# Optimization experiments

Hardware: AMD Instinct MI355X
Metric: run time of the kernel (lower is better)

Reference implementation:

```python
import jax, jax.numpy as jnp
import numpy as np

N_NODES = 50000
N_EDGES = 800000
IN_FEATS, H_FEATS, N_CLASSES = 64, 64, 16


def setup_inputs() -> dict:
    key = jax.random.key(0)
    ks = jax.random.split(key, 8)
    x = jax.random.normal(ks[0], (N_NODES, IN_FEATS), dtype=jnp.float32)
    src = jax.random.randint(ks[1], (N_EDGES,), 0, N_NODES, dtype=jnp.int64)
    dst = jax.random.randint(ks[2], (N_EDGES,), 0, N_NODES, dtype=jnp.int64)
    W_self1 = jax.random.normal(ks[3], (IN_FEATS, H_FEATS), dtype=jnp.float32) / np.sqrt(IN_FEATS)
    W_neigh1 = jax.random.normal(ks[4], (IN_FEATS, H_FEATS), dtype=jnp.float32) / np.sqrt(IN_FEATS)
    b1 = jnp.zeros((H_FEATS,), dtype=jnp.float32)
    W_self2 = jax.random.normal(ks[5], (H_FEATS, N_CLASSES), dtype=jnp.float32) / np.sqrt(H_FEATS)
    W_neigh2 = jax.random.normal(ks[6], (H_FEATS, N_CLASSES), dtype=jnp.float32) / np.sqrt(H_FEATS)
    b2 = jnp.zeros((N_CLASSES,), dtype=jnp.float32)
    return {"x": x, "src": src, "dst": dst,
            "W_self1": W_self1, "W_neigh1": W_neigh1, "b1": b1,
            "W_self2": W_self2, "W_neigh2": W_neigh2, "b2": b2}


def _mean_agg(h, src, dst, n_nodes):
    # gather source-node features along edges, sum into destinations, divide by in-degree
    summed = jax.ops.segment_sum(h[src], dst, num_segments=n_nodes)  # [N, d]
    deg = jax.ops.segment_sum(jnp.ones_like(src, dtype=h.dtype), dst, num_segments=n_nodes)
    return summed / jnp.maximum(deg, 1.0)[:, None]  # zero in-degree -> zeros (DGL semantics)


def _sage_layer(h, src, dst, W_self, W_neigh, b):
    h_neigh = _mean_agg(h, src, dst, h.shape[0])
    return h @ W_self + h_neigh @ W_neigh + b


def reference(x, src, dst, W_self1, W_neigh1, b1, W_self2, W_neigh2, b2):
    h = _sage_layer(x, src, dst, W_self1, W_neigh1, b1)
    h = jax.nn.relu(h)
    out = _sage_layer(h, src, dst, W_self2, W_neigh2, b2)
    return out
```

## Files before the change

kernel.cpp:

```cpp
#include <hip/hip_runtime.h>
#include <hip/hip_bf16.h>
#include <cstring>


#define FEATS 64
#define CLS   16
#define EPT   16
#define CAP   5120
#define CAPN  64

typedef unsigned short bf16_t;
typedef float floatx2 __attribute__((ext_vector_type(2)));

__device__ __forceinline__ float bfbits2f(unsigned lo16) {
    unsigned v = lo16 << 16;
    float f;
    __builtin_memcpy(&f, &v, 4);
    return f;
}
__device__ __forceinline__ bf16_t f2bf(float f) {
    unsigned u;
    __builtin_memcpy(&u, &f, 4);
    u = (u + 0x7FFFu + ((u >> 16) & 1u)) >> 16;
    return (bf16_t)u;
}
__device__ __forceinline__ unsigned pack2(float a, float b) {
    return (unsigned)f2bf(a) | ((unsigned)f2bf(b) << 16);
}
__device__ __forceinline__ unsigned pack4_fp8(float a, float b, float c, float d) {
    int q = __builtin_amdgcn_cvt_pk_fp8_f32(a, b, 0, false);
    q = __builtin_amdgcn_cvt_pk_fp8_f32(c, d, q, true);
    return (unsigned)q;
}

__global__ __launch_bounds__(256) void fused_pg_kernel(
    const int* __restrict__ src, const int* __restrict__ dst,
    int* __restrict__ bucket_cnt, int* __restrict__ epart, int E,
    const float* __restrict__ x, const float* __restrict__ Ws,
    const float* __restrict__ Wn, bf16_t* __restrict__ selfo,
    unsigned char* __restrict__ t1, int N, int nbp)
{
    __shared__ float smem[16512];
    int t = threadIdx.x;

    if ((int)blockIdx.x < nbp) {
        int* hist = (int*)smem;
        int* base = hist + 256;
        int e0 = blockIdx.x * (256 * EPT);
        hist[t] = 0;
        __syncthreads();
        int pk[EPT];
        int bk[EPT];
#pragma unroll
        for (int j = 0; j < EPT; ++j) {
            int e = e0 + j * 256 + t;
            if (e < E) {
                int d = dst[e];
                pk[j] = (src[e] << 8) | (d & 255);
                bk[j] = d >> 8;
                atomicAdd(&hist[bk[j]], 1);
            } else bk[j] = -1;
        }
        __syncthreads();
        int c = hist[t];
        if (c) base[t] = atomicAdd(&bucket_cnt[t], c);
        hist[t] = 0;
        __syncthreads();
#pragma unroll
        for (int j = 0; j < EPT; ++j) {
            if (bk[j] >= 0) {
                int r = atomicAdd(&hist[bk[j]], 1);
                epart[bk[j] * CAP + base[bk[j]] + r] = pk[j];
            }
        }
        return;
    }

    float* Wc = smem;
    float* xs = smem + 8192;
    int node0 = ((int)blockIdx.x - nbp) * 128;

    for (int idx = t; idx < 64 * 128; idx += 256) {
        int k = idx >> 7, c = idx & 127;
        Wc[idx] = (c < 64) ? Ws[k * 64 + c] : Wn[k * 64 + (c - 64)];
    }
    for (int idx = t; idx < 128 * 16; idx += 256) {
        int row = idx >> 4, c4 = idx & 15;
        int node = node0 + row;
        float4 v = (node < N) ? ((const float4*)(x + (size_t)node * 64))[c4]
                              : make_float4(0.f, 0.f, 0.f, 0.f);
        float* p = &xs[row * 65 + c4 * 4];
        p[0] = v.x; p[1] = v.y; p[2] = v.z; p[3] = v.w;
    }
    __syncthreads();

    int m = t & 31;
    int g = t >> 5;
    float acc[4][16];
#pragma unroll
    for (int j = 0; j < 4; ++j)
#pragma unroll
        for (int c = 0; c < 16; ++c) acc[j][c] = 0.f;

    for (int k = 0; k < 64; ++k) {
        float w[16];
        const float* wp = &Wc[k * 128 + g * 16];
#pragma unroll
        for (int c = 0; c < 16; ++c) w[c] = wp[c];
        float a0 = xs[m * 65 + k];
        float a1 = xs[(m + 32) * 65 + k];
        float a2 = xs[(m + 64) * 65 + k];
        float a3 = xs[(m + 96) * 65 + k];
#pragma unroll
        for (int c = 0; c < 16; ++c) {
            acc[0][c] += a0 * w[c];
            acc[1][c] += a1 * w[c];
            acc[2][c] += a2 * w[c];
            acc[3][c] += a3 * w[c];
        }
    }
#pragma unroll
    for (int j = 0; j < 4; ++j) {
        int node = node0 + m + 32 * j;
        if (node < N) {
            if (g < 4) {
                bf16_t* dstp = selfo + (size_t)node * 64 + g * 16;
                uint4 p0, p1;
                p0.x = pack2(acc[j][0],  acc[j][1]);  p0.y = pack2(acc[j][2],  acc[j][3]);
                p0.z = pack2(acc[j][4],  acc[j][5]);  p0.w = pack2(acc[j][6],  acc[j][7]);
                p1.x = pack2(acc[j][8],  acc[j][9]);  p1.y = pack2(acc[j][10], acc[j][11]);
                p1.z = pack2(acc[j][12], acc[j][13]); p1.w = pack2(acc[j][14], acc[j][15]);
                *(uint4*)(dstp) = p0;
                *(uint4*)(dstp + 8) = p1;
            } else {
                unsigned char* dstp = t1 + (size_t)node * 64 + (g - 4) * 16;
                uint4 q;
                q.x = pack4_fp8(acc[j][0],  acc[j][1],  acc[j][2],  acc[j][3]);
                q.y = pack4_fp8(acc[j][4],  acc[j][5],  acc[j][6],  acc[j][7]);
                q.z = pack4_fp8(acc[j][8],  acc[j][9],  acc[j][10], acc[j][11]);
                q.w = pack4_fp8(acc[j][12], acc[j][13], acc[j][14], acc[j][15]);
                *(uint4*)(dstp) = q;
            }
        }
    }
}

__global__ __launch_bounds__(256) void buildcsr_kernel(const int* __restrict__ epart,
                                                       const int* __restrict__ bucket_cnt,
                                                       int* __restrict__ cnt,
                                                       int* __restrict__ csr, int N) {
    __shared__ int c[256];
    int t = threadIdx.x;
    int b = blockIdx.x;
    int ebeg = b * CAP;
    int ecnt = bucket_cnt[b];
    c[t] = 0;
    __syncthreads();
    for (int e = t; e < ecnt; e += 256) {
        int pk = epart[ebeg + e];
        int ln = pk & 255;
        int r = atomicAdd(&c[ln], 1);
        if (r < CAPN) csr[(size_t)(b * 256 + ln) * CAPN + r] = pk >> 8;
    }
    __syncthreads();
    int node = b * 256 + t;
    if (node < N) cnt[node] = c[t];
}

__global__ __launch_bounds__(256) void gather64_kernel(
    const int* __restrict__ csr, const int* __restrict__ cnt,
    const unsigned char* __restrict__ t1, const bf16_t* __restrict__ selfo,
    bf16_t* __restrict__ h1, const float* __restrict__ b1, int N)
{
    int wid = (blockIdx.x * 256 + threadIdx.x) >> 6;
    int lane = threadIdx.x & 63;
    int eslot = lane >> 4;
    int cg = lane & 15;
    if (wid >= N) return;
    int eraw = csr[(size_t)wid * CAPN + lane];
    int d = cnt[wid];
    size_t o = (size_t)wid * 64 + cg * 4;
    uint2 su;
    float4 bb;
    if (eslot == 0) {
        su = *(const uint2*)(selfo + o);
        bb = *(const float4*)(b1 + cg * 4);
    }
    d = min(d, CAPN);
    float ax = 0.f, ay = 0.f, az = 0.f, aw = 0.f;
    if (d > 0) {
        int dm1 = d - 1;
#define G64_ACC(r, m)                                                      \
        {                                                                  \
            floatx2 p_ = __builtin_amdgcn_cvt_pk_f32_fp8((int)(r), false); \
            floatx2 q_ = __builtin_amdgcn_cvt_pk_f32_fp8((int)(r), true);  \
            ax += (m) * p_.x; ay += (m) * p_.y;                            \
            az += (m) * q_.x; aw += (m) * q_.y;                            \
        }
#define G64_BATCH(KN)                                                      \
        {                                                                  \
            int ss[KN];                                                    \
            float mk[KN];                                                  \
            unsigned rr[KN];                                               \
            _Pragma("unroll")                                              \
            for (int k = 0; k < KN; ++k) {                                 \
                int i = eslot + 4 * k;                                     \
                int idx = i > dm1 ? dm1 : i;                               \
                mk[k] = (i <= dm1) ? 1.f : 0.f;                            \
                ss[k] = __shfl(eraw, idx);                                 \
            }                                                              \
            _Pragma("unroll")                                              \
            for (int k = 0; k < KN; ++k)                                   \
                rr[k] = *(const unsigned*)(t1 + (size_t)ss[k] * 64 + cg * 4); \
            _Pragma("unroll")                                              \
            for (int k = 0; k < KN; ++k) G64_ACC(rr[k], mk[k]);            \
        }
        if (d <= 16) {
            G64_BATCH(4)
        } else if (d <= 32) {
            G64_BATCH(8)
        } else {
            G64_BATCH(16)
        }
#undef G64_BATCH
#undef G64_ACC
        ax += __shfl_xor(ax, 16); ay += __shfl_xor(ay, 16);
        az += __shfl_xor(az, 16); aw += __shfl_xor(aw, 16);
        ax += __shfl_xor(ax, 32); ay += __shfl_xor(ay, 32);
        az += __shfl_xor(az, 32); aw += __shfl_xor(aw, 32);
    }
    if (eslot == 0) {
        float inv = 1.f / fmaxf((float)d, 1.f);
        float rx = fmaxf(bfbits2f(su.x & 0xffff) + ax * inv + bb.x, 0.f);
        float ry = fmaxf(bfbits2f(su.x >> 16)    + ay * inv + bb.y, 0.f);
        float rz = fmaxf(bfbits2f(su.y & 0xffff) + az * inv + bb.z, 0.f);
        float rw = fmaxf(bfbits2f(su.y >> 16)    + aw * inv + bb.w, 0.f);
        uint2 pk;
        pk.x = pack2(rx, ry);
        pk.y = pack2(rz, rw);
        *(uint2*)(h1 + o) = pk;
    }
}

__global__ __launch_bounds__(256) void gather16_kernel(
    const int* __restrict__ csr, const int* __restrict__ cnt,
    const bf16_t* __restrict__ t2,
    float* __restrict__ outp, const float* __restrict__ b2, int N)
{
    int wid = (blockIdx.x * 256 + threadIdx.x) >> 6;
    int lane = threadIdx.x & 63;
    int eslot = lane >> 3;
    int c2 = lane & 7;
    if (wid >= N) return;
    int eraw = csr[(size_t)wid * CAPN + lane];
    int d = cnt[wid];
    size_t o = (size_t)wid * 16 + c2 * 2;
    float2 oo = make_float2(0.f, 0.f), bbv = make_float2(0.f, 0.f);
    if (eslot == 0) {
        oo = *(const float2*)(outp + o);
        bbv = *(const float2*)(b2 + c2 * 2);
    }
    d = min(d, CAPN);
    float a0 = 0.f, a1 = 0.f;
    if (d > 0) {
        int dm1 = d - 1;
#define G16_BATCH(KN)                                                      \
        {                                                                  \
            int ss[KN];                                                    \
            float mk[KN];                                                  \
            unsigned uu[KN];                                               \
            _Pragma("unroll")                                              \
            for (int k = 0; k < KN; ++k) {                                 \
                int i = eslot + 8 * k;                                     \
                int idx = i > dm1 ? dm1 : i;                               \
                mk[k] = (i <= dm1) ? 1.f : 0.f;                            \
                ss[k] = __shfl(eraw, idx);                                 \
            }                                                              \
            _Pragma("unroll")                                              \
            for (int k = 0; k < KN; ++k)                                   \
                uu[k] = *(const unsigned*)(t2 + (size_t)ss[k] * 16 + c2 * 2); \
            _Pragma("unroll")                                              \
            for (int k = 0; k < KN; ++k) {                                 \
                a0 += mk[k] * bfbits2f(uu[k] & 0xffff);                    \
                a1 += mk[k] * bfbits2f(uu[k] >> 16);                       \
            }                                                              \
        }
        if (d <= 16) {
            G16_BATCH(2)
        } else if (d <= 32) {
            G16_BATCH(4)
        } else {
            G16_BATCH(8)
        }
#undef G16_BATCH
        a0 += __shfl_xor(a0, 8);  a1 += __shfl_xor(a1, 8);
        a0 += __shfl_xor(a0, 16); a1 += __shfl_xor(a1, 16);
        a0 += __shfl_xor(a0, 32); a1 += __shfl_xor(a1, 32);
    }
    if (eslot == 0) {
        float inv = 1.f / fmaxf((float)d, 1.f);
        float2 r;
        r.x = oo.x + a0 * inv + bbv.x;
        r.y = oo.y + a1 * inv + bbv.y;
        *(float2*)(outp + o) = r;
    }
}

__global__ __launch_bounds__(256) void gemm2_kernel(
    const bf16_t* __restrict__ h1, const float* __restrict__ Ws,
    const float* __restrict__ Wn, float* __restrict__ outp,
    bf16_t* __restrict__ t2, int N)
{
    __shared__ float Wc[64 * 32];
    __shared__ float xs[128 * 65];
    int t = threadIdx.x;
    int node0 = blockIdx.x * 128;

    for (int idx = t; idx < 64 * 32; idx += 256) {
        int k = idx >> 5, c = idx & 31;
        Wc[idx] = (c < 16) ? Ws[k * 16 + c] : Wn[k * 16 + (c - 16)];
    }
    for (int idx = t; idx < 128 * 8; idx += 256) {
        int row = idx >> 3, c8 = idx & 7;
        int node = node0 + row;
        float* p = &xs[row * 65 + c8 * 8];
        if (node < N) {
            uint4 u = *(const uint4*)(h1 + (size_t)node * 64 + c8 * 8);
            p[0] = bfbits2f(u.x & 0xffff); p[1] = bfbits2f(u.x >> 16);
            p[2] = bfbits2f(u.y & 0xffff); p[3] = bfbits2f(u.y >> 16);
            p[4] = bfbits2f(u.z & 0xffff); p[5] = bfbits2f(u.z >> 16);
            p[6] = bfbits2f(u.w & 0xffff); p[7] = bfbits2f(u.w >> 16);
        } else {
            for (int qq = 0; qq < 8; ++qq) p[qq] = 0.f;
        }
    }
    __syncthreads();

    int m = t & 31;
    int g = t >> 5;
    float acc[4][4];
#pragma unroll
    for (int j = 0; j < 4; ++j)
#pragma unroll
        for (int c = 0; c < 4; ++c) acc[j][c] = 0.f;

    for (int k = 0; k < 64; ++k) {
        float w[4];
        const float* wp = &Wc[k * 32 + g * 4];
#pragma unroll
        for (int c = 0; c < 4; ++c) w[c] = wp[c];
        float a0 = xs[m * 65 + k];
        float a1 = xs[(m + 32) * 65 + k];
        float a2 = xs[(m + 64) * 65 + k];
        float a3 = xs[(m + 96) * 65 + k];
#pragma unroll
        for (int c = 0; c < 4; ++c) {
            acc[0][c] += a0 * w[c];
            acc[1][c] += a1 * w[c];
            acc[2][c] += a2 * w[c];
            acc[3][c] += a3 * w[c];
        }
    }
#pragma unroll
    for (int j = 0; j < 4; ++j) {
        int node = node0 + m + 32 * j;
        if (node < N) {
            if (g < 4) {
                *(float4*)(outp + (size_t)node * 16 + g * 4) =
                    make_float4(acc[j][0], acc[j][1], acc[j][2], acc[j][3]);
            } else {
                uint2 pk;
                pk.x = pack2(acc[j][0], acc[j][1]);
                pk.y = pack2(acc[j][2], acc[j][3]);
                *(uint2*)(t2 + (size_t)node * 16 + (g - 4) * 4) = pk;
            }
        }
    }
}

extern "C" void kernel_launch(void* const* d_in, const int* in_sizes, int n_in,
                              void* d_out, int out_size, void* d_ws, size_t ws_size,
                              hipStream_t stream) {
    const float* x   = (const float*)d_in[0];
    const int*   src = (const int*)d_in[1];
    const int*   dst = (const int*)d_in[2];
    const float* Ws1 = (const float*)d_in[3];
    const float* Wn1 = (const float*)d_in[4];
    const float* b1  = (const float*)d_in[5];
    const float* Ws2 = (const float*)d_in[6];
    const float* Wn2 = (const float*)d_in[7];
    const float* b2  = (const float*)d_in[8];
    float* outp = (float*)d_out;

    const int N = in_sizes[0] / FEATS;
    const int E = in_sizes[1];
    const int B = (N + 255) / 256;
    const int NBP = (E + 256 * EPT - 1) / (256 * EPT);
    const int NBG = (N + 127) / 128;

    char* p = (char*)d_ws;
    auto align16 = [](char* q) { return (char*)(((size_t)q + 15) & ~(size_t)15); };
    int* bucket_cnt    = (int*)p;                  p = (char*)(bucket_cnt + 256);
    int* epart         = (int*)p;                  p = (char*)(epart + (size_t)B * CAP);
    int* cnt           = (int*)align16(p);         p = (char*)(cnt + N);
    int* csr           = (int*)align16(p);         p = (char*)(csr + (size_t)N * CAPN);
    bf16_t* selfo      = (bf16_t*)align16(p);      p = (char*)(selfo + (size_t)N * 64);
    unsigned char* t1  = (unsigned char*)align16(p); p = (char*)(t1 + (size_t)N * 64);
    bf16_t* h1         = (bf16_t*)align16(p);      p = (char*)(h1 + (size_t)N * 64);
    bf16_t* t2         = (bf16_t*)align16(p);

    hipMemsetAsync(bucket_cnt, 0, 256 * sizeof(int), stream);

    fused_pg_kernel<<<NBP + NBG, 256, 0, stream>>>(
        src, dst, bucket_cnt, epart, E, x, Ws1, Wn1, selfo, t1, N, NBP);
    buildcsr_kernel<<<B, 256, 0, stream>>>(epart, bucket_cnt, cnt, csr, N);

    gather64_kernel<<<((size_t)N * 64 + 255) / 256, 256, 0, stream>>>(
        csr, cnt, t1, selfo, h1, b1, N);
    gemm2_kernel<<<(N + 127) / 128, 256, 0, stream>>>(h1, Ws2, Wn2, outp, t2, N);
    gather16_kernel<<<((size_t)N * 64 + 255) / 256, 256, 0, stream>>>(
        csr, cnt, t2, outp, b2, N);
}
```

Measured before the change: 152.5 us.

## Split CSR build across chunked blocks with global atomics and 16-bit indices

```diff
diff --git a/kernel.cpp b/kernel.cpp
--- a/kernel.cpp
+++ b/kernel.cpp
@@ -8,6 +8,7 @@
 #define EPT   16
 #define CAP   5120
 #define CAPN  64
+#define BCHUNK 1024
 
 typedef unsigned short bf16_t;
 typedef float floatx2 __attribute__((ext_vector_type(2)));
@@ -148,27 +149,24 @@
 __global__ __launch_bounds__(256) void buildcsr_kernel(const int* __restrict__ epart,
                                                        const int* __restrict__ bucket_cnt,
                                                        int* __restrict__ cnt,
-                                                       int* __restrict__ csr, int N) {
-    __shared__ int c[256];
-    int t = threadIdx.x;
+                                                       unsigned short* __restrict__ csr,
+                                                       int N) {
     int b = blockIdx.x;
+    int ecnt = bucket_cnt[b];
+    int start = blockIdx.y * BCHUNK;
+    int end = start + BCHUNK;
+    if (end > ecnt) end = ecnt;
     int ebeg = b * CAP;
-    int ecnt = bucket_cnt[b];
-    c[t] = 0;
-    __syncthreads();
-    for (int e = t; e < ecnt; e += 256) {
+    for (int e = start + (int)threadIdx.x; e < end; e += 256) {
         int pk = epart[ebeg + e];
-        int ln = pk & 255;
-        int r = atomicAdd(&c[ln], 1);
-        if (r < CAPN) csr[(size_t)(b * 256 + ln) * CAPN + r] = pk >> 8;
-    }
-    __syncthreads();
-    int node = b * 256 + t;
-    if (node < N) cnt[node] = c[t];
+        int node = b * 256 + (pk & 255);
+        int r = atomicAdd(&cnt[node], 1);
+        if (r < CAPN) csr[(size_t)node * CAPN + r] = (unsigned short)(pk >> 8);
+    }
 }
 
 __global__ __launch_bounds__(256) void gather64_kernel(
-    const int* __restrict__ csr, const int* __restrict__ cnt,
+    const unsigned short* __restrict__ csr, const int* __restrict__ cnt,
     const unsigned char* __restrict__ t1, const bf16_t* __restrict__ selfo,
     bf16_t* __restrict__ h1, const float* __restrict__ b1, int N)
 {
@@ -243,7 +241,7 @@
 }
 
 __global__ __launch_bounds__(256) void gather16_kernel(
-    const int* __restrict__ csr, const int* __restrict__ cnt,
+    const unsigned short* __restrict__ csr, const int* __restrict__ cnt,
     const bf16_t* __restrict__ t2,
     float* __restrict__ outp, const float* __restrict__ b2, int N)
 {
@@ -266,9 +264,7 @@
         int dm1 = d - 1;
 #define G16_BATCH(KN)                                                      \
         {                                                                  \
-            int ss[KN];                                                    \
-            float mk[KN];                                                  \
-            unsigned uu[KN];                                               \
+            int ss[KN]; float mk[KN]; unsigned uu[KN];                     \
             _Pragma("unroll")                                              \
             for (int k = 0; k < KN; ++k) {                                 \
                 int i = eslot + 8 * k;                                     \
@@ -401,19 +397,20 @@
     char* p = (char*)d_ws;
     auto align16 = [](char* q) { return (char*)(((size_t)q + 15) & ~(size_t)15); };
     int* bucket_cnt    = (int*)p;                  p = (char*)(bucket_cnt + 256);
-    int* epart         = (int*)p;                  p = (char*)(epart + (size_t)B * CAP);
-    int* cnt           = (int*)align16(p);         p = (char*)(cnt + N);
-    int* csr           = (int*)align16(p);         p = (char*)(csr + (size_t)N * CAPN);
+    int* cnt           = (int*)p;                  p = (char*)(cnt + N);
+    int* epart         = (int*)align16(p);         p = (char*)(epart + (size_t)B * CAP);
+    unsigned short* csr = (unsigned short*)align16(p); p = (char*)(csr + (size_t)N * CAPN);
     bf16_t* selfo      = (bf16_t*)align16(p);      p = (char*)(selfo + (size_t)N * 64);
     unsigned char* t1  = (unsigned char*)align16(p); p = (char*)(t1 + (size_t)N * 64);
     bf16_t* h1         = (bf16_t*)align16(p);      p = (char*)(h1 + (size_t)N * 64);
     bf16_t* t2         = (bf16_t*)align16(p);
 
-    hipMemsetAsync(bucket_cnt, 0, 256 * sizeof(int), stream);
+    hipMemsetAsync(bucket_cnt, 0, (256 + (size_t)N) * sizeof(int), stream);
 
     fused_pg_kernel<<<NBP + NBG, 256, 0, stream>>>(
         src, dst, bucket_cnt, epart, E, x, Ws1, Wn1, selfo, t1, N, NBP);
-    buildcsr_kernel<<<B, 256, 0, stream>>>(epart, bucket_cnt, cnt, csr, N);
+    buildcsr_kernel<<<dim3(B, (CAP + BCHUNK - 1) / BCHUNK), 256, 0, stream>>>(
+        epart, bucket_cnt, cnt, csr, N);
 
     gather64_kernel<<<((size_t)N * 64 + 255) / 256, 256, 0, stream>>>(
         csr, cnt, t1, selfo, h1, b1, N);
```

Result: slower. 160.3 us (+5.1%).

## Fuse layer-2 GEMM into neighbor gather and use per-block edge partition slots

Applied to the files above, without the earlier changes.

```diff
diff --git a/kernel.cpp b/kernel.cpp
--- a/kernel.cpp
+++ b/kernel.cpp
@@ -6,7 +6,7 @@
 #define FEATS 64
 #define CLS   16
 #define EPT   16
-#define CAP   5120
+#define CAPB  64
 #define CAPN  64
 
 typedef unsigned short bf16_t;
@@ -18,6 +18,18 @@
     __builtin_memcpy(&f, &v, 4);
     return f;
 }
+__device__ __forceinline__ float bf_lo(unsigned u) {
+    unsigned v = u << 16;
+    float f;
+    __builtin_memcpy(&f, &v, 4);
+    return f;
+}
+__device__ __forceinline__ float bf_hi(unsigned u) {
+    unsigned v = u & 0xffff0000u;
+    float f;
+    __builtin_memcpy(&f, &v, 4);
+    return f;
+}
 __device__ __forceinline__ bf16_t f2bf(float f) {
     unsigned u;
     __builtin_memcpy(&u, &f, 4);
@@ -35,7 +47,7 @@
 
 __global__ __launch_bounds__(256) void fused_pg_kernel(
     const int* __restrict__ src, const int* __restrict__ dst,
-    int* __restrict__ bucket_cnt, int* __restrict__ epart, int E,
+    int* __restrict__ blkcnt, int* __restrict__ epart, int E,
     const float* __restrict__ x, const float* __restrict__ Ws,
     const float* __restrict__ Wn, bf16_t* __restrict__ selfo,
     unsigned char* __restrict__ t1, int N, int nbp)
@@ -45,34 +57,23 @@
 
     if ((int)blockIdx.x < nbp) {
         int* hist = (int*)smem;
-        int* base = hist + 256;
         int e0 = blockIdx.x * (256 * EPT);
         hist[t] = 0;
         __syncthreads();
-        int pk[EPT];
-        int bk[EPT];
 #pragma unroll
         for (int j = 0; j < EPT; ++j) {
             int e = e0 + j * 256 + t;
             if (e < E) {
                 int d = dst[e];
-                pk[j] = (src[e] << 8) | (d & 255);
-                bk[j] = d >> 8;
-                atomicAdd(&hist[bk[j]], 1);
-            } else bk[j] = -1;
+                int pk = (src[e] << 8) | (d & 255);
+                int bk = d >> 8;
+                int r = atomicAdd(&hist[bk], 1);
+                if (r < CAPB)
+                    epart[((size_t)bk * nbp + blockIdx.x) * CAPB + r] = pk;
+            }
         }
         __syncthreads();
-        int c = hist[t];
-        if (c) base[t] = atomicAdd(&bucket_cnt[t], c);
-        hist[t] = 0;
-        __syncthreads();
-#pragma unroll
-        for (int j = 0; j < EPT; ++j) {
-            if (bk[j] >= 0) {
-                int r = atomicAdd(&hist[bk[j]], 1);
-                epart[bk[j] * CAP + base[bk[j]] + r] = pk[j];
-            }
-        }
+        blkcnt[(size_t)blockIdx.x * 256 + t] = hist[t];
         return;
     }
 
@@ -146,25 +147,31 @@
 }
 
 __global__ __launch_bounds__(256) void buildcsr_kernel(const int* __restrict__ epart,
-                                                       const int* __restrict__ bucket_cnt,
+                                                       const int* __restrict__ blkcnt,
                                                        int* __restrict__ cnt,
-                                                       int* __restrict__ csr, int N) {
-    __shared__ int c[256];
+                                                       int* __restrict__ csr,
+                                                       int N, int nbp) {
+    __shared__ int cseg[256];
+    __shared__ int nodecnt[256];
     int t = threadIdx.x;
     int b = blockIdx.x;
-    int ebeg = b * CAP;
-    int ecnt = bucket_cnt[b];
-    c[t] = 0;
+    cseg[t] = (t < nbp) ? blkcnt[(size_t)t * 256 + b] : 0;
+    nodecnt[t] = 0;
     __syncthreads();
-    for (int e = t; e < ecnt; e += 256) {
-        int pk = epart[ebeg + e];
-        int ln = pk & 255;
-        int r = atomicAdd(&c[ln], 1);
-        if (r < CAPN) csr[(size_t)(b * 256 + ln) * CAPN + r] = pk >> 8;
+    int total = nbp * CAPB;
+    for (int idx = t; idx < total; idx += 256) {
+        int i = idx >> 6;
+        int r = idx & 63;
+        if (r < cseg[i]) {
+            int pk = epart[((size_t)b * nbp + i) * CAPB + r];
+            int ln = pk & 255;
+            int s = atomicAdd(&nodecnt[ln], 1);
+            if (s < CAPN) csr[(size_t)(b * 256 + ln) * CAPN + s] = pk >> 8;
+        }
     }
     __syncthreads();
     int node = b * 256 + t;
-    if (node < N) cnt[node] = c[t];
+    if (node < N) cnt[node] = nodecnt[t];
 }
 
 __global__ __launch_bounds__(256) void gather64_kernel(
@@ -242,139 +249,96 @@
     }
 }
 
-__global__ __launch_bounds__(256) void gather16_kernel(
+__global__ __launch_bounds__(256) void gather16f_kernel(
     const int* __restrict__ csr, const int* __restrict__ cnt,
-    const bf16_t* __restrict__ t2,
-    float* __restrict__ outp, const float* __restrict__ b2, int N)
+    const bf16_t* __restrict__ h1,
+    const float* __restrict__ Ws2, const float* __restrict__ Wn2,
+    const float* __restrict__ b2, float* __restrict__ outp, int N)
 {
     int wid = (blockIdx.x * 256 + threadIdx.x) >> 6;
     int lane = threadIdx.x & 63;
-    int eslot = lane >> 3;
+    int ks = lane >> 3;
     int c2 = lane & 7;
     if (wid >= N) return;
     int eraw = csr[(size_t)wid * CAPN + lane];
     int d = cnt[wid];
-    size_t o = (size_t)wid * 16 + c2 * 2;
-    float2 oo = make_float2(0.f, 0.f), bbv = make_float2(0.f, 0.f);
-    if (eslot == 0) {
-        oo = *(const float2*)(outp + o);
-        bbv = *(const float2*)(b2 + c2 * 2);
-    }
+    uint4 own = *(const uint4*)(h1 + (size_t)wid * 64 + ks * 8);
+    float ws[8][2], wn[8][2];
+#pragma unroll
+    for (int k = 0; k < 8; ++k) {
+        float2 a = *(const float2*)(Ws2 + (ks * 8 + k) * 16 + c2 * 2);
+        float2 q = *(const float2*)(Wn2 + (ks * 8 + k) * 16 + c2 * 2);
+        ws[k][0] = a.x; ws[k][1] = a.y;
+        wn[k][0] = q.x; wn[k][1] = q.y;
+    }
+    float2 bbv = *(const float2*)(b2 + c2 * 2);
     d = min(d, CAPN);
-    float a0 = 0.f, a1 = 0.f;
+    float agg[8];
+#pragma unroll
+    for (int k = 0; k < 8; ++k) agg[k] = 0.f;
     if (d > 0) {
         int dm1 = d - 1;
-#define G16_BATCH(KN)                                                      \
+#define G16F_BATCH(KB)                                                     \
         {                                                                  \
-            int ss[KN];                                                    \
-            float mk[KN];                                                  \
-            unsigned uu[KN];                                               \
-            _Pragma("unroll")                                              \
-            for (int k = 0; k < KN; ++k) {                                 \
-                int i = eslot + 8 * k;                                     \
-                int idx = i > dm1 ? dm1 : i;                               \
-                mk[k] = (i <= dm1) ? 1.f : 0.f;                            \
-                ss[k] = __shfl(eraw, idx);                                 \
+            uint4 vv[8]; float mk[8];                                      \
+            _Pragma("unroll")                                              \
+            for (int q = 0; q < 8; ++q) {                                  \
+                int i = (KB) * 8 + q;                                      \
+                int ix = i > dm1 ? dm1 : i;                                \
+                mk[q] = (i <= dm1) ? 1.f : 0.f;                            \
+                int nb = __shfl(eraw, ix);                                 \
+                vv[q] = *(const uint4*)(h1 + (size_t)nb * 64 + ks * 8);    \
             }                                                              \
             _Pragma("unroll")                                              \
-            for (int k = 0; k < KN; ++k)                                   \
-                uu[k] = *(const unsigned*)(t2 + (size_t)ss[k] * 16 + c2 * 2); \
-            _Pragma("unroll")                                              \
-            for (int k = 0; k < KN; ++k) {                                 \
-                a0 += mk[k] * bfbits2f(uu[k] & 0xffff);                    \
-                a1 += mk[k] * bfbits2f(uu[k] >> 16);                       \
+            for (int q = 0; q < 8; ++q) {                                  \
+                float m = mk[q]; uint4 v = vv[q];                          \
+                agg[0] += m * bf_lo(v.x); agg[1] += m * bf_hi(v.x);        \
+                agg[2] += m * bf_lo(v.y); agg[3] += m * bf_hi(v.y);        \
+                agg[4] += m * bf_lo(v.z); agg[5] += m * bf_hi(v.z);        \
+                agg[6] += m * bf_lo(v.w); agg[7] += m * bf_hi(v.w);        \
             }                                                              \
         }
-        if (d <= 16) {
-            G16_BATCH(2)
+        if (d <= 8) {
+            G16F_BATCH(0)
+        } else if (d <= 16) {
+            G16F_BATCH(0) G16F_BATCH(1)
         } else if (d <= 32) {
-            G16_BATCH(4)
+            G16F_BATCH(0) G16F_BATCH(1) G16F_BATCH(2) G16F_BATCH(3)
         } else {
-            G16_BATCH(8)
-        }
-#undef G16_BATCH
-        a0 += __shfl_xor(a0, 8);  a1 += __shfl_xor(a1, 8);
-        a0 += __shfl_xor(a0, 16); a1 += __shfl_xor(a1, 16);
-        a0 += __shfl_xor(a0, 32); a1 += __shfl_xor(a1, 32);
-    }
-    if (eslot == 0) {
-        float inv = 1.f / fmaxf((float)d, 1.f);
+            for (int i = 0; i < d; ++i) {
+                int nb = __shfl(eraw, i);
+                uint4 v = *(const uint4*)(h1 + (size_t)nb * 64 + ks * 8);
+                agg[0] += bf_lo(v.x); agg[1] += bf_hi(v.x);
+                agg[2] += bf_lo(v.y); agg[3] += bf_hi(v.y);
+                agg[4] += bf_lo(v.z); agg[5] += bf_hi(v.z);
+                agg[6] += bf_lo(v.w); agg[7] += bf_hi(v.w);
+            }
+        }
+#undef G16F_BATCH
+    }
+    float inv = 1.f / fmaxf((float)d, 1.f);
+    float p0 = 0.f, p1 = 0.f;
+    {
+        float hv, av;
+        unsigned uu[4] = {own.x, own.y, own.z, own.w};
+#pragma unroll
+        for (int k = 0; k < 4; ++k) {
+            hv = bf_lo(uu[k]); av = agg[2 * k] * inv;
+            p0 += hv * ws[2 * k][0] + av * wn[2 * k][0];
+            p1 += hv * ws[2 * k][1] + av * wn[2 * k][1];
+            hv = bf_hi(uu[k]); av = agg[2 * k + 1] * inv;
+            p0 += hv * ws[2 * k + 1][0] + av * wn[2 * k + 1][0];
+            p1 += hv * ws[2 * k + 1][1] + av * wn[2 * k + 1][1];
+        }
+    }
+    p0 += __shfl_xor(p0, 8);  p1 += __shfl_xor(p1, 8);
+    p0 += __shfl_xor(p0, 16); p1 += __shfl_xor(p1, 16);
+    p0 += __shfl_xor(p0, 32); p1 += __shfl_xor(p1, 32);
+    if (ks == 0) {
         float2 r;
-        r.x = oo.x + a0 * inv + bbv.x;
-        r.y = oo.y + a1 * inv + bbv.y;
-        *(float2*)(outp + o) = r;
-    }
-}
-
-__global__ __launch_bounds__(256) void gemm2_kernel(
-    const bf16_t* __restrict__ h1, const float* __restrict__ Ws,
-    const float* __restrict__ Wn, float* __restrict__ outp,
-    bf16_t* __restrict__ t2, int N)
-{
-    __shared__ float Wc[64 * 32];
-    __shared__ float xs[128 * 65];
-    int t = threadIdx.x;
-    int node0 = blockIdx.x * 128;
-
-    for (int idx = t; idx < 64 * 32; idx += 256) {
-        int k = idx >> 5, c = idx & 31;
-        Wc[idx] = (c < 16) ? Ws[k * 16 + c] : Wn[k * 16 + (c - 16)];
-    }
-    for (int idx = t; idx < 128 * 8; idx += 256) {
-        int row = idx >> 3, c8 = idx & 7;
-        int node = node0 + row;
-        float* p = &xs[row * 65 + c8 * 8];
-        if (node < N) {
-            uint4 u = *(const uint4*)(h1 + (size_t)node * 64 + c8 * 8);
-            p[0] = bfbits2f(u.x & 0xffff); p[1] = bfbits2f(u.x >> 16);
-            p[2] = bfbits2f(u.y & 0xffff); p[3] = bfbits2f(u.y >> 16);
-            p[4] = bfbits2f(u.z & 0xffff); p[5] = bfbits2f(u.z >> 16);
-            p[6] = bfbits2f(u.w & 0xffff); p[7] = bfbits2f(u.w >> 16);
-        } else {
-            for (int qq = 0; qq < 8; ++qq) p[qq] = 0.f;
-        }
-    }
-    __syncthreads();
-
-    int m = t & 31;
-    int g = t >> 5;
-    float acc[4][4];
-#pragma unroll
-    for (int j = 0; j < 4; ++j)
-#pragma unroll
-        for (int c = 0; c < 4; ++c) acc[j][c] = 0.f;
-
-    for (int k = 0; k < 64; ++k) {
-        float w[4];
-        const float* wp = &Wc[k * 32 + g * 4];
-#pragma unroll
-        for (int c = 0; c < 4; ++c) w[c] = wp[c];
-        float a0 = xs[m * 65 + k];
-        float a1 = xs[(m + 32) * 65 + k];
-        float a2 = xs[(m + 64) * 65 + k];
-        float a3 = xs[(m + 96) * 65 + k];
-#pragma unroll
-        for (int c = 0; c < 4; ++c) {
-            acc[0][c] += a0 * w[c];
-            acc[1][c] += a1 * w[c];
-            acc[2][c] += a2 * w[c];
-            acc[3][c] += a3 * w[c];
-        }
-    }
-#pragma unroll
-    for (int j = 0; j < 4; ++j) {
-        int node = node0 + m + 32 * j;
-        if (node < N) {
-            if (g < 4) {
-                *(float4*)(outp + (size_t)node * 16 + g * 4) =
-                    make_float4(acc[j][0], acc[j][1], acc[j][2], acc[j][3]);
-            } else {
-                uint2 pk;
-                pk.x = pack2(acc[j][0], acc[j][1]);
-                pk.y = pack2(acc[j][2], acc[j][3]);
-                *(uint2*)(t2 + (size_t)node * 16 + (g - 4) * 4) = pk;
-            }
-        }
+        r.x = p0 + bbv.x;
+        r.y = p1 + bbv.y;
+        *(float2*)(outp + (size_t)wid * 16 + c2 * 2) = r;
     }
 }
 
@@ -400,24 +364,20 @@
 
     char* p = (char*)d_ws;
     auto align16 = [](char* q) { return (char*)(((size_t)q + 15) & ~(size_t)15); };
-    int* bucket_cnt    = (int*)p;                  p = (char*)(bucket_cnt + 256);
-    int* epart         = (int*)p;                  p = (char*)(epart + (size_t)B * CAP);
+    int* blkcnt        = (int*)p;                  p = (char*)(blkcnt + (size_t)NBP * 256);
+    int* epart         = (int*)align16(p);         p = (char*)(epart + (size_t)B * NBP * CAPB);
     int* cnt           = (int*)align16(p);         p = (char*)(cnt + N);
     int* csr           = (int*)align16(p);         p = (char*)(csr + (size_t)N * CAPN);
     bf16_t* selfo      = (bf16_t*)align16(p);      p = (char*)(selfo + (size_t)N * 64);
     unsigned char* t1  = (unsigned char*)align16(p); p = (char*)(t1 + (size_t)N * 64);
-    bf16_t* h1         = (bf16_t*)align16(p);      p = (char*)(h1 + (size_t)N * 64);
-    bf16_t* t2         = (bf16_t*)align16(p);
-
-    hipMemsetAsync(bucket_cnt, 0, 256 * sizeof(int), stream);
+    bf16_t* h1         = (bf16_t*)align16(p);
 
     fused_pg_kernel<<<NBP + NBG, 256, 0, stream>>>(
-        src, dst, bucket_cnt, epart, E, x, Ws1, Wn1, selfo, t1, N, NBP);
-    buildcsr_kernel<<<B, 256, 0, stream>>>(epart, bucket_cnt, cnt, csr, N);
+        src, dst, blkcnt, epart, E, x, Ws1, Wn1, selfo, t1, N, NBP);
+    buildcsr_kernel<<<B, 256, 0, stream>>>(epart, blkcnt, cnt, csr, N, NBP);
 
     gather64_kernel<<<((size_t)N * 64 + 255) / 256, 256, 0, stream>>>(
         csr, cnt, t1, selfo, h1, b1, N);
-    gemm2_kernel<<<(N + 127) / 128, 256, 0, stream>>>(h1, Ws2, Wn2, outp, t2, N);
-    gather16_kernel<<<((size_t)N * 64 + 255) / 256, 256, 0, stream>>>(
-        csr, cnt, t2, outp, b2, N);
-}
+    gather16f_kernel<<<((size_t)N * 64 + 255) / 256, 256, 0, stream>>>(
+        csr, cnt, h1, Ws2, Wn2, b2, outp, N);
+}
```

New measurement: 217.9 us. 1.43x slower.

## Fuse CSR build with layer-1 GEMM and store CSR indices as 16-bit

Applied to the files above, without the earlier changes.

```diff
diff --git a/kernel.cpp b/kernel.cpp
--- a/kernel.cpp
+++ b/kernel.cpp
@@ -33,52 +33,79 @@
     return (unsigned)q;
 }
 
-__global__ __launch_bounds__(256) void fused_pg_kernel(
+__global__ __launch_bounds__(256) void partition_kernel(
     const int* __restrict__ src, const int* __restrict__ dst,
-    int* __restrict__ bucket_cnt, int* __restrict__ epart, int E,
+    int* __restrict__ bucket_cnt, int* __restrict__ epart, int E)
+{
+    __shared__ int hist[256];
+    __shared__ int base[256];
+    int t = threadIdx.x;
+    int e0 = blockIdx.x * (256 * EPT);
+    hist[t] = 0;
+    __syncthreads();
+    int pk[EPT];
+    int bk[EPT];
+#pragma unroll
+    for (int j = 0; j < EPT; ++j) {
+        int e = e0 + j * 256 + t;
+        if (e < E) {
+            int d = dst[e];
+            pk[j] = (src[e] << 8) | (d & 255);
+            bk[j] = d >> 8;
+            atomicAdd(&hist[bk[j]], 1);
+        } else bk[j] = -1;
+    }
+    __syncthreads();
+    int c = hist[t];
+    if (c) base[t] = atomicAdd(&bucket_cnt[t], c);
+    hist[t] = 0;
+    __syncthreads();
+#pragma unroll
+    for (int j = 0; j < EPT; ++j) {
+        if (bk[j] >= 0) {
+            int r = atomicAdd(&hist[bk[j]], 1);
+            epart[bk[j] * CAP + base[bk[j]] + r] = pk[j];
+        }
+    }
+}
+
+__global__ __launch_bounds__(256) void fused_bg_kernel(
+    const int* __restrict__ epart, const int* __restrict__ bucket_cnt,
+    int* __restrict__ cnt, unsigned short* __restrict__ csr,
     const float* __restrict__ x, const float* __restrict__ Ws,
     const float* __restrict__ Wn, bf16_t* __restrict__ selfo,
-    unsigned char* __restrict__ t1, int N, int nbp)
+    unsigned char* __restrict__ t1, int N, int nbg)
 {
     __shared__ float smem[16512];
     int t = threadIdx.x;
 
-    if ((int)blockIdx.x < nbp) {
-        int* hist = (int*)smem;
-        int* base = hist + 256;
-        int e0 = blockIdx.x * (256 * EPT);
-        hist[t] = 0;
+    if ((int)blockIdx.x >= nbg) {
+        int u = (int)blockIdx.x - nbg;
+        int b = u >> 2;
+        int q = u & 3;
+        int* c = (int*)smem;
+        if (t < 64) c[t] = 0;
         __syncthreads();
-        int pk[EPT];
-        int bk[EPT];
-#pragma unroll
-        for (int j = 0; j < EPT; ++j) {
-            int e = e0 + j * 256 + t;
-            if (e < E) {
-                int d = dst[e];
-                pk[j] = (src[e] << 8) | (d & 255);
-                bk[j] = d >> 8;
-                atomicAdd(&hist[bk[j]], 1);
-            } else bk[j] = -1;
+        int ebeg = b * CAP;
+        int ecnt = bucket_cnt[b];
+        for (int e = t; e < ecnt; e += 256) {
+            int pk = epart[ebeg + e];
+            int ln = pk & 255;
+            if ((ln >> 6) == q) {
+                int r = atomicAdd(&c[ln & 63], 1);
+                if (r < CAPN)
+                    csr[(size_t)(b * 256 + ln) * CAPN + r] = (unsigned short)(pk >> 8);
+            }
         }
         __syncthreads();
-        int c = hist[t];
-        if (c) base[t] = atomicAdd(&bucket_cnt[t], c);
-        hist[t] = 0;
-        __syncthreads();
-#pragma unroll
-        for (int j = 0; j < EPT; ++j) {
-            if (bk[j] >= 0) {
-                int r = atomicAdd(&hist[bk[j]], 1);
-                epart[bk[j] * CAP + base[bk[j]] + r] = pk[j];
-            }
-        }
+        int node = b * 256 + q * 64 + t;
+        if (t < 64 && node < N) cnt[node] = c[t];
         return;
     }
 
     float* Wc = smem;
     float* xs = smem + 8192;
-    int node0 = ((int)blockIdx.x - nbp) * 128;
+    int node0 = (int)blockIdx.x * 128;
 
     for (int idx = t; idx < 64 * 128; idx += 256) {
         int k = idx >> 7, c = idx & 127;
@@ -134,41 +161,19 @@
                 *(uint4*)(dstp + 8) = p1;
             } else {
                 unsigned char* dstp = t1 + (size_t)node * 64 + (g - 4) * 16;
-                uint4 q;
-                q.x = pack4_fp8(acc[j][0],  acc[j][1],  acc[j][2],  acc[j][3]);
-                q.y = pack4_fp8(acc[j][4],  acc[j][5],  acc[j][6],  acc[j][7]);
-                q.z = pack4_fp8(acc[j][8],  acc[j][9],  acc[j][10], acc[j][11]);
-                q.w = pack4_fp8(acc[j][12], acc[j][13], acc[j][14], acc[j][15]);
-                *(uint4*)(dstp) = q;
+                uint4 qv;
+                qv.x = pack4_fp8(acc[j][0],  acc[j][1],  acc[j][2],  acc[j][3]);
+                qv.y = pack4_fp8(acc[j][4],  acc[j][5],  acc[j][6],  acc[j][7]);
+                qv.z = pack4_fp8(acc[j][8],  acc[j][9],  acc[j][10], acc[j][11]);
+                qv.w = pack4_fp8(acc[j][12], acc[j][13], acc[j][14], acc[j][15]);
+                *(uint4*)(dstp) = qv;
             }
         }
     }
 }
 
-__global__ __launch_bounds__(256) void buildcsr_kernel(const int* __restrict__ epart,
-                                                       const int* __restrict__ bucket_cnt,
-                                                       int* __restrict__ cnt,
-                                                       int* __restrict__ csr, int N) {
-    __shared__ int c[256];
-    int t = threadIdx.x;
-    int b = blockIdx.x;
-    int ebeg = b * CAP;
-    int ecnt = bucket_cnt[b];
-    c[t] = 0;
-    __syncthreads();
-    for (int e = t; e < ecnt; e += 256) {
-        int pk = epart[ebeg + e];
-        int ln = pk & 255;
-        int r = atomicAdd(&c[ln], 1);
-        if (r < CAPN) csr[(size_t)(b * 256 + ln) * CAPN + r] = pk >> 8;
-    }
-    __syncthreads();
-    int node = b * 256 + t;
-    if (node < N) cnt[node] = c[t];
-}
-
 __global__ __launch_bounds__(256) void gather64_kernel(
-    const int* __restrict__ csr, const int* __restrict__ cnt,
+    const unsigned short* __restrict__ csr, const int* __restrict__ cnt,
     const unsigned char* __restrict__ t1, const bf16_t* __restrict__ selfo,
     bf16_t* __restrict__ h1, const float* __restrict__ b1, int N)
 {
@@ -177,7 +182,7 @@
     int eslot = lane >> 4;
     int cg = lane & 15;
     if (wid >= N) return;
-    int eraw = csr[(size_t)wid * CAPN + lane];
+    int eraw = (int)csr[(size_t)wid * CAPN + lane];
     int d = cnt[wid];
     size_t o = (size_t)wid * 64 + cg * 4;
     uint2 su;
@@ -239,70 +244,6 @@
         pk.x = pack2(rx, ry);
         pk.y = pack2(rz, rw);
         *(uint2*)(h1 + o) = pk;
-    }
-}
-
-__global__ __launch_bounds__(256) void gather16_kernel(
-    const int* __restrict__ csr, const int* __restrict__ cnt,
-    const bf16_t* __restrict__ t2,
-    float* __restrict__ outp, const float* __restrict__ b2, int N)
-{
-    int wid = (blockIdx.x * 256 + threadIdx.x) >> 6;
-    int lane = threadIdx.x & 63;
-    int eslot = lane >> 3;
-    int c2 = lane & 7;
-    if (wid >= N) return;
-    int eraw = csr[(size_t)wid * CAPN + lane];
-    int d = cnt[wid];
-    size_t o = (size_t)wid * 16 + c2 * 2;
-    float2 oo = make_float2(0.f, 0.f), bbv = make_float2(0.f, 0.f);
-    if (eslot == 0) {
-        oo = *(const float2*)(outp + o);
-        bbv = *(const float2*)(b2 + c2 * 2);
-    }
-    d = min(d, CAPN);
-    float a0 = 0.f, a1 = 0.f;
-    if (d > 0) {
-        int dm1 = d - 1;
-#define G16_BATCH(KN)                                                      \
-        {                                                                  \
-            int ss[KN];                                                    \
-            float mk[KN];                                                  \
-            unsigned uu[KN];                                               \
-            _Pragma("unroll")                                              \
-            for (int k = 0; k < KN; ++k) {                                 \
-                int i = eslot + 8 * k;                                     \
-                int idx = i > dm1 ? dm1 : i;                               \
-                mk[k] = (i <= dm1) ? 1.f : 0.f;                            \
-                ss[k] = __shfl(eraw, idx);                                 \
-            }                                                              \
-            _Pragma("unroll")                                              \
-            for (int k = 0; k < KN; ++k)                                   \
-                uu[k] = *(const unsigned*)(t2 + (size_t)ss[k] * 16 + c2 * 2); \
-            _Pragma("unroll")                                              \
-            for (int k = 0; k < KN; ++k) {                                 \
-                a0 += mk[k] * bfbits2f(uu[k] & 0xffff);                    \
-                a1 += mk[k] * bfbits2f(uu[k] >> 16);                       \
-            }                                                              \
-        }
-        if (d <= 16) {
-            G16_BATCH(2)
-        } else if (d <= 32) {
-            G16_BATCH(4)
-        } else {
-            G16_BATCH(8)
-        }
-#undef G16_BATCH
-        a0 += __shfl_xor(a0, 8);  a1 += __shfl_xor(a1, 8);
-        a0 += __shfl_xor(a0, 16); a1 += __shfl_xor(a1, 16);
-        a0 += __shfl_xor(a0, 32); a1 += __shfl_xor(a1, 32);
-    }
-    if (eslot == 0) {
-        float inv = 1.f / fmaxf((float)d, 1.f);
-        float2 r;
-        r.x = oo.x + a0 * inv + bbv.x;
-        r.y = oo.y + a1 * inv + bbv.y;
-        *(float2*)(outp + o) = r;
     }
 }
 
@@ -375,6 +316,68 @@
                 *(uint2*)(t2 + (size_t)node * 16 + (g - 4) * 4) = pk;
             }
         }
+    }
+}
+
+__global__ __launch_bounds__(256) void gather16_kernel(
+    const unsigned short* __restrict__ csr, const int* __restrict__ cnt,
+    const bf16_t* __restrict__ t2,
+    float* __restrict__ outp, const float* __restrict__ b2, int N)
+{
+    int wid = (blockIdx.x * 256 + threadIdx.x) >> 6;
+    int lane = threadIdx.x & 63;
+    int eslot = lane >> 3;
+    int c2 = lane & 7;
+    if (wid >= N) return;
+    int eraw = (int)csr[(size_t)wid * CAPN + lane];
+    int d = cnt[wid];
+    size_t o = (size_t)wid * 16 + c2 * 2;
+    float2 oo = make_float2(0.f, 0.f), bbv = make_float2(0.f, 0.f);
+    if (eslot == 0) {
+        oo = *(const float2*)(outp + o);
+        bbv = *(const float2*)(b2 + c2 * 2);
+    }
+    d = min(d, CAPN);
+    float a0 = 0.f, a1 = 0.f;
+    if (d > 0) {
+        int dm1 = d - 1;
+#define G16_BATCH(KN)                                                      \
+        {                                                                  \
+            int ss[KN]; float mk[KN]; unsigned uu[KN];                     \
+            _Pragma("unroll")                                              \
+            for (int k = 0; k < KN; ++k) {                                 \
+                int i = eslot + 8 * k;                                     \
+                int idx = i > dm1 ? dm1 : i;                               \
+                mk[k] = (i <= dm1) ? 1.f : 0.f;                            \
+                ss[k] = __shfl(eraw, idx);                                 \
+            }                                                              \
+            _Pragma("unroll")                                              \
+            for (int k = 0; k < KN; ++k)                                   \
+                uu[k] = *(const unsigned*)(t2 + (size_t)ss[k] * 16 + c2 * 2); \
+            _Pragma("unroll")                                              \
+            for (int k = 0; k < KN; ++k) {                                 \
+                a0 += mk[k] * bfbits2f(uu[k] & 0xffff);                    \
+                a1 += mk[k] * bfbits2f(uu[k] >> 16);                       \
+            }                                                              \
+        }
+        if (d <= 16) {
+            G16_BATCH(2)
+        } else if (d <= 32) {
+            G16_BATCH(4)
+        } else {
+            G16_BATCH(8)
+        }
+#undef G16_BATCH
+        a0 += __shfl_xor(a0, 8);  a1 += __shfl_xor(a1, 8);
+        a0 += __shfl_xor(a0, 16); a1 += __shfl_xor(a1, 16);
+        a0 += __shfl_xor(a0, 32); a1 += __shfl_xor(a1, 32);
+    }
+    if (eslot == 0) {
+        float inv = 1.f / fmaxf((float)d, 1.f);
+        float2 r;
+        r.x = oo.x + a0 * inv + bbv.x;
+        r.y = oo.y + a1 * inv + bbv.y;
+        *(float2*)(outp + o) = r;
     }
 }
 
@@ -403,7 +406,7 @@
     int* bucket_cnt    = (int*)p;                  p = (char*)(bucket_cnt + 256);
     int* epart         = (int*)p;                  p = (char*)(epart + (size_t)B * CAP);
     int* cnt           = (int*)align16(p);         p = (char*)(cnt + N);
-    int* csr           = (int*)align16(p);         p = (char*)(csr + (size_t)N * CAPN);
+    unsigned short* csr = (unsigned short*)align16(p); p = (char*)(csr + (size_t)N * CAPN);
     bf16_t* selfo      = (bf16_t*)align16(p);      p = (char*)(selfo + (size_t)N * 64);
     unsigned char* t1  = (unsigned char*)align16(p); p = (char*)(t1 + (size_t)N * 64);
     bf16_t* h1         = (bf16_t*)align16(p);      p = (char*)(h1 + (size_t)N * 64);
@@ -411,9 +414,9 @@
 
     hipMemsetAsync(bucket_cnt, 0, 256 * sizeof(int), stream);
 
-    fused_pg_kernel<<<NBP + NBG, 256, 0, stream>>>(
-        src, dst, bucket_cnt, epart, E, x, Ws1, Wn1, selfo, t1, N, NBP);
-    buildcsr_kernel<<<B, 256, 0, stream>>>(epart, bucket_cnt, cnt, csr, N);
+    partition_kernel<<<NBP, 256, 0, stream>>>(src, dst, bucket_cnt, epart, E);
+    fused_bg_kernel<<<NBG + 4 * B, 256, 0, stream>>>(
+        epart, bucket_cnt, cnt, csr, x, Ws1, Wn1, selfo, t1, N, NBG);
 
     gather64_kernel<<<((size_t)N * 64 + 255) / 256, 256, 0, stream>>>(
         csr, cnt, t1, selfo, h1, b1, N);
```

After: 156.9 us. 2.8% more time.
